# Performance work log

Hardware: AMD Instinct MI355X
Metric: run time of the kernel (lower is better)

The kernel has to match this reference:

```python
import jax, jax.numpy as jnp
import numpy as np
from jax import lax

B, CIN, COUT, K, MOD, BANK = 4, 64, 32, 3, 128, 4
D = H = W = 32
EPS = 1e-8


def _lin_upsample2x(x, axis):
    n = x.shape[axis]
    dst = jnp.arange(2 * n, dtype=jnp.float32)
    src = jnp.maximum((dst + 0.5) * 0.5 - 0.5, 0.0)
    i0 = jnp.floor(src).astype(jnp.int32)
    i1 = jnp.minimum(i0 + 1, n - 1)
    w1 = src - i0.astype(jnp.float32)
    shape = [1] * x.ndim
    shape[axis] = 2 * n
    w1 = w1.reshape(shape)
    return jnp.take(x, i0, axis=axis) * (1.0 - w1) + jnp.take(x, i1, axis=axis) * w1


def upsample_trilinear2x(x):
    for ax in (2, 3, 4):
        x = _lin_upsample2x(x, ax)
    return x


def setup_inputs() -> dict:
    key = jax.random.key(0)
    ks = jax.random.split(key, 9)
    fan = CIN * K * K * K
    return {
        "x": jax.random.normal(ks[0], (B, CIN, D, H, W), jnp.float32),
        "style": jax.random.normal(ks[1], (B, MOD), jnp.float32),
        "bank": jax.random.normal(ks[2], (BANK, COUT, CIN, K, K, K), jnp.float32) / np.sqrt(fan),
        "affine_w": jax.random.normal(ks[3], (CIN, MOD), jnp.float32) / np.sqrt(MOD),
        "affine_b": jnp.ones((CIN,), jnp.float32),  # StyleGAN bias init = 1
        "sel_w": jax.random.normal(ks[4], (BANK, MOD), jnp.float32) / np.sqrt(MOD),
        "sel_b": jnp.zeros((BANK,), jnp.float32),
        "vox_w": jax.random.normal(ks[5], (1, COUT), jnp.float32) / np.sqrt(COUT),
        "vox_b": jnp.zeros((1,), jnp.float32),
    }


def reference(x, style, bank, affine_w, affine_b, sel_w, sel_b, vox_w, vox_b):
    # --- AdaptiveModulatedConv3d: select kernel from bank, modulate, demodulate ---
    alpha = jax.nn.softmax(style @ sel_w.T + sel_b, axis=-1)            # [B, BANK]
    w = jnp.einsum('bn,noidhw->boidhw', alpha, bank)                    # per-sample kernel
    s = style @ affine_w.T + affine_b                                   # [B, CIN]
    w = w * s[:, None, :, None, None, None]                             # modulate
    demod = lax.rsqrt(jnp.sum(w * w, axis=(2, 3, 4, 5)) + EPS)          # [B, COUT]
    w = w * demod[:, :, None, None, None, None]

    def conv1(xi, wi):
        return lax.conv_general_dilated(
            xi[None], wi, window_strides=(1, 1, 1),
            padding=[(1, 1), (1, 1), (1, 1)],
            dimension_numbers=('NCDHW', 'OIDHW', 'NCDHW'))[0]

    y = jax.vmap(conv1)(x, w)                                           # [B, COUT, D, H, W]

    y = upsample_trilinear2x(y)                                         # [B, COUT, 2D, 2H, 2W]

    # --- VoxelizingBlock: 1x1x1 conv to 1 channel ---
    out = jnp.einsum('oc,bcdhw->bodhw', vox_w, y) + vox_b[None, :, None, None, None]
    return (y, out)
```

## Files before the change

### kernel.cpp

```cpp
#include <hip/hip_runtime.h>
#include <math.h>

#define B_    4
#define CIN_  64
#define COUT_ 32
#define MOD_  128
#define VOX_  32768
#define UPVOX_ 262144
#define TAPS_ 27
#define EPS_  1e-8f

#define HALO_   1224
#define XUNITS_ 2448
#define WUNITS_ 1728
#define CHUNK_HALVES_ 13824

#define WS_ALPHA 0
#define WS_S     16
#define WS_WF16  512
#define WS_Y     111104
#define WS_V32   4305408

#define OUT_YUP  0
#define OUT_VOX  33554432

typedef _Float16 half8 __attribute__((ext_vector_type(8)));
typedef float floatx16 __attribute__((ext_vector_type(16)));

__global__ __launch_bounds__(256) void k_style(
    const float* __restrict__ style,
    const float* __restrict__ affine_w,
    const float* __restrict__ affine_b,
    const float* __restrict__ sel_w,
    const float* __restrict__ sel_b,
    float* __restrict__ ws) {
  __shared__ float lg[16];
  const int tid = threadIdx.x;

  if (tid < 16) {
    const int b = tid >> 2, n = tid & 3;
    float l = sel_b[n];
    for (int k = 0; k < MOD_; ++k) l += style[b * MOD_ + k] * sel_w[n * MOD_ + k];
    lg[tid] = l;
  }
  __syncthreads();
  if (tid < 16) {
    const int b = tid >> 2;
    const float m = fmaxf(fmaxf(lg[b * 4 + 0], lg[b * 4 + 1]),
                          fmaxf(lg[b * 4 + 2], lg[b * 4 + 3]));
    float den = 0.f;
    for (int j = 0; j < 4; ++j) den += expf(lg[b * 4 + j] - m);
    ws[WS_ALPHA + tid] = expf(lg[tid] - m) / den;
  }
  {
    const int b = tid >> 6, i = tid & 63;
    float v = affine_b[i];
    for (int k = 0; k < MOD_; ++k) v += style[b * MOD_ + k] * affine_w[i * MOD_ + k];
    ws[WS_S + tid] = v;
  }
}

__global__ __launch_bounds__(256) void k_weights(
    const float* __restrict__ bank,
    const float* __restrict__ ws_in,
    _Float16* __restrict__ wf) {
  const int b = blockIdx.x >> 5;
  const int o = blockIdx.x & 31;
  const int tid = threadIdx.x;
  __shared__ float red[256];

  float al[4];
#pragma unroll
  for (int n = 0; n < 4; ++n) al[n] = ws_in[WS_ALPHA + b * 4 + n];
  const float* sB = ws_in + WS_S + b * 64;

  float wv[7];
  float ss = 0.f;
#pragma unroll
  for (int r = 0; r < 7; ++r) {
    const int e = tid + r * 256;
    float v = 0.f;
    if (e < CIN_ * TAPS_) {
      const int i = e / TAPS_;
      const int t = e - i * TAPS_;
      const int base = (o * CIN_ + i) * TAPS_ + t;
      float bw = 0.f;
#pragma unroll
      for (int n = 0; n < 4; ++n)
        bw += al[n] * bank[base + n * (COUT_ * CIN_ * TAPS_)];
      v = bw * sB[i];
    }
    wv[r] = v;
    ss += v * v;
  }
  red[tid] = ss;
  __syncthreads();
  for (int st = 128; st > 0; st >>= 1) {
    if (tid < st) red[tid] += red[tid + st];
    __syncthreads();
  }
  const float demod = rsqrtf(red[0] + EPS_);

#pragma unroll
  for (int r = 0; r < 7; ++r) {
    const int e = tid + r * 256;
    if (e < CIN_ * TAPS_) {
      const int i = e / TAPS_;
      const int t = e - i * TAPS_;
      const int c = i >> 4, h = (i >> 3) & 1, j = i & 7;
      wf[((((b * 4 + c) * TAPS_ + t) * 2 + h) * 32 + o) * 8 + j] =
          (_Float16)(wv[r] * demod);
    }
  }
}

__global__ __launch_bounds__(256) void k_pack(
    const float* __restrict__ x, _Float16* __restrict__ xt) {
  const int yp = blockIdx.x, zp = blockIdx.y, b = blockIdx.z;
  const int gz = zp - 1, gy = yp - 1;
  const bool zy_ok = ((unsigned)gz < 32u) && ((unsigned)gy < 32u);
  const int gzc = min(max(gz, 0), 31);
  const int gyc = min(max(gy, 0), 31);
  _Float16* dst = xt + (((size_t)(b * 34 + zp) * 34 + yp) * 34) * 64;
  const float* srow = x + ((size_t)b * CIN_) * VOX_ + gzc * 1024 + gyc * 32;
  for (int u = threadIdx.x; u < 34 * 8; u += 256) {
    const int xp = u >> 3, q = u & 7;
    const int gx = xp - 1;
    const bool ok = zy_ok && ((unsigned)gx < 32u);
    const float m = ok ? 1.0f : 0.0f;
    const int gxc = min(max(gx, 0), 31);
    half8 h;
#pragma unroll
    for (int i = 0; i < 8; ++i) {
      const float v = srow[(size_t)(q * 8 + i) * VOX_ + gxc];
      h[i] = (_Float16)(v * m);
    }
    *(half8*)&dst[xp * 64 + q * 8] = h;
  }
}

__global__ __launch_bounds__(256, 1) void k_conv(
    const _Float16* __restrict__ xt,
    const _Float16* __restrict__ wf,
    const float* __restrict__ vox_w,
    float* __restrict__ ws_y,
    float* __restrict__ v32) {
  __shared__ __align__(16) _Float16 wl[2][CHUNK_HALVES_];
  __shared__ __align__(16) _Float16 xs[2][XUNITS_ * 8];

  const int b  = blockIdx.y;
  const int bx = blockIdx.x;
  const int z0 = (bx >> 3) * 4;
  const int y0 = (bx & 7) * 4;
  const int tid = threadIdx.x;
  const int w = tid >> 6;
  const int lane = tid & 63;
  const int hf = lane >> 5;
  const int col = lane & 31;
  const int wz = (w >> 1) * 2;
  const int wy = (w & 1) * 2;

  const _Float16* xtb = xt + (size_t)b * (34 * 34 * 34 * 64);
  const _Float16* wfb = wf + (size_t)b * 4 * CHUNK_HALVES_;

  int xoff[10];
  bool xok[10];
#pragma unroll
  for (int j = 0; j < 10; ++j) {
    const int u = j * 256 + tid;
    xok[j] = (u < XUNITS_);
    const int uc = xok[j] ? u : 0;
    const int h = uc / HALO_, hv = uc - h * HALO_;
    const int hz = hv / 204;
    const int rem = hv - hz * 204;
    const int hy = rem / 34;
    const int hx = rem - hy * 34;
    xoff[j] = (((z0 + hz) * 34 + (y0 + hy)) * 34 + hx) * 64 + h * 8;
  }

  floatx16 acc[2][2];
#pragma unroll
  for (int az = 0; az < 2; ++az)
#pragma unroll
    for (int ay = 0; ay < 2; ++ay)
#pragma unroll
      for (int r = 0; r < 16; ++r) acc[az][ay][r] = 0.f;

  half8 wv[7], xv[10];

  auto load_chunk = [&](int c) {
    const _Float16* wsrc = wfb + (size_t)c * CHUNK_HALVES_;
#pragma unroll
    for (int j = 0; j < 7; ++j) {
      const int u = j * 256 + tid;
      wv[j] = *(const half8*)(wsrc + (size_t)(u < WUNITS_ ? u : 0) * 8);
    }
#pragma unroll
    for (int j = 0; j < 10; ++j)
      xv[j] = *(const half8*)(xtb + xoff[j] + c * 16);
  };
  auto write_chunk = [&](int bufi) {
#pragma unroll
    for (int j = 0; j < 7; ++j) {
      const int u = j * 256 + tid;
      if (u < WUNITS_) *(half8*)&wl[bufi][u * 8] = wv[j];
    }
#pragma unroll
    for (int j = 0; j < 10; ++j) {
      const int u = j * 256 + tid;
      if (xok[j]) *(half8*)&xs[bufi][u * 8] = xv[j];
    }
  };
  auto compute = [&](int bufi) {
    const _Float16* xb_ = xs[bufi];
    const _Float16* wb_ = wl[bufi];
#pragma unroll
    for (int dx = 0; dx < 3; ++dx) {
      half8 Bf[4][4];
#pragma unroll
      for (int zs = 0; zs < 4; ++zs)
#pragma unroll
        for (int ys = 0; ys < 4; ++ys) {
          const int hv = ((wz + zs) * 6 + (wy + ys)) * 34 + dx + col;
          Bf[zs][ys] = *(const half8*)&xb_[(hf * HALO_ + hv) * 8];
        }
#pragma unroll
      for (int dz = 0; dz < 3; ++dz)
#pragma unroll
        for (int dy = 0; dy < 3; ++dy) {
          const int t = (dz * 3 + dy) * 3 + dx;
          const half8 af = *(const half8*)&wb_[((t * 2 + hf) * 32 + col) * 8];
          acc[0][0] = __builtin_amdgcn_mfma_f32_32x32x16_f16(af, Bf[dz][dy], acc[0][0], 0, 0, 0);
          acc[0][1] = __builtin_amdgcn_mfma_f32_32x32x16_f16(af, Bf[dz][dy + 1], acc[0][1], 0, 0, 0);
          acc[1][0] = __builtin_amdgcn_mfma_f32_32x32x16_f16(af, Bf[dz + 1][dy], acc[1][0], 0, 0, 0);
          acc[1][1] = __builtin_amdgcn_mfma_f32_32x32x16_f16(af, Bf[dz + 1][dy + 1], acc[1][1], 0, 0, 0);
        }
    }
  };

  load_chunk(0);
  write_chunk(0);
  __syncthreads();
  for (int c = 0; c < 4; ++c) {
    if (c < 3) load_chunk(c + 1);
    compute(c & 1);
    if (c < 3) {
      write_chunk((c + 1) & 1);
      __syncthreads();
    }
  }

  float vw[16];
#pragma unroll
  for (int r = 0; r < 16; ++r)
    vw[r] = vox_w[(r & 3) + 8 * (r >> 2) + 4 * hf];

  float* yb2 = ws_y + (size_t)b * COUT_ * VOX_;
#pragma unroll
  for (int az = 0; az < 2; ++az)
#pragma unroll
    for (int ay = 0; ay < 2; ++ay) {
      const int zz = z0 + wz + az, yy = y0 + wy + ay;
      const int vbase = zz * 1024 + yy * 32 + col;
      float p = 0.f;
#pragma unroll
      for (int r = 0; r < 16; ++r) {
        const int oc = (r & 3) + 8 * (r >> 2) + 4 * hf;
        yb2[(size_t)oc * VOX_ + vbase] = acc[az][ay][r];
        p = fmaf(vw[r], acc[az][ay][r], p);
      }
      p += __shfl_xor(p, 32);
      if (hf == 0) v32[((size_t)b << 15) + vbase] = p;
    }
}

__global__ __launch_bounds__(256) void k_up(
    const float* __restrict__ ws_y,
    const float* __restrict__ v32,
    const float* __restrict__ vox_b,
    float* __restrict__ out) {
  __shared__ float P[3][1056];
  const int kz = blockIdx.x;
  const int ch = blockIdx.y;
  const int b = blockIdx.z;

  const int pzm = max(kz - 1, 0), pzp = min(kz + 1, 31);
  const float* src = (ch < 32) ? (ws_y + (((size_t)(b * 32 + ch)) << 15))
                               : (v32 + ((size_t)b << 15));
  for (int j = threadIdx.x; j < 768; j += 256) {
    const int p = j >> 8, idx = j & 255;
    const int r = idx >> 3, q = (idx & 7) * 4;
    const int zsrc = (p == 0) ? pzm : ((p == 1) ? kz : pzp);
    const float4 v = *(const float4*)(src + (zsrc << 10) + r * 32 + q);
    float* dp = &P[p][r * 33 + q];
    dp[0] = v.x; dp[1] = v.y; dp[2] = v.z; dp[3] = v.w;
  }
  __syncthreads();

  const int yp = threadIdx.x >> 3;
  const int xq = threadIdx.x & 7;
  const int ym = max(yp - 1, 0) * 33, yc = yp * 33, ypp = min(yp + 1, 31) * 33;

  int gxi[6];
#pragma unroll
  for (int i = 0; i < 6; ++i) gxi[i] = min(max(4 * xq - 1 + i, 0), 31);

  float ry[3][2][6];
#pragma unroll
  for (int p = 0; p < 3; ++p)
#pragma unroll
    for (int i = 0; i < 6; ++i) {
      const float a = P[p][ym + gxi[i]];
      const float bb = P[p][yc + gxi[i]];
      const float cc = P[p][ypp + gxi[i]];
      ry[p][0][i] = fmaf(0.25f, a, 0.75f * bb);
      ry[p][1][i] = fmaf(0.25f, cc, 0.75f * bb);
    }

  const float vb = (ch == 32) ? vox_b[0] : 0.f;
  float* base = out + ((ch < 32) ? (OUT_YUP + (((size_t)(b * 32 + ch)) * UPVOX_))
                                 : (OUT_VOX + (size_t)b * UPVOX_)) +
                (size_t)(2 * kz) * 4096 + (2 * yp) * 64 + 8 * xq;

#pragma unroll
  for (int zo = 0; zo < 2; ++zo)
#pragma unroll
    for (int yo = 0; yo < 2; ++yo) {
      float s[6];
#pragma unroll
      for (int i = 0; i < 6; ++i)
        s[i] = zo == 0 ? fmaf(0.25f, ry[0][yo][i], 0.75f * ry[1][yo][i])
                       : fmaf(0.25f, ry[2][yo][i], 0.75f * ry[1][yo][i]);
      float o[8];
#pragma unroll
      for (int ox = 0; ox < 8; ++ox) {
        const int k = ox >> 1;
        o[ox] = (ox & 1) ? fmaf(0.25f, s[k + 2], 0.75f * s[k + 1])
                         : fmaf(0.25f, s[k], 0.75f * s[k + 1]);
        o[ox] += vb;
      }
      float4* dst = (float4*)(base + (size_t)zo * 4096 + yo * 64);
      float4 v0; v0.x = o[0]; v0.y = o[1]; v0.z = o[2]; v0.w = o[3];
      float4 v1; v1.x = o[4]; v1.y = o[5]; v1.z = o[6]; v1.w = o[7];
      dst[0] = v0;
      dst[1] = v1;
    }
}

extern "C" void kernel_launch(void* const* d_in, const int* in_sizes, int n_in,
                              void* d_out, int out_size, void* d_ws, size_t ws_size,
                              hipStream_t stream) {
  const float* x        = (const float*)d_in[0];
  const float* style    = (const float*)d_in[1];
  const float* bank     = (const float*)d_in[2];
  const float* affine_w = (const float*)d_in[3];
  const float* affine_b = (const float*)d_in[4];
  const float* sel_w    = (const float*)d_in[5];
  const float* sel_b    = (const float*)d_in[6];
  const float* vox_w    = (const float*)d_in[7];
  const float* vox_b    = (const float*)d_in[8];
  float* out = (float*)d_out;
  float* ws  = (float*)d_ws;
  _Float16* wf16 = (_Float16*)(ws + WS_WF16);
  float* ws_y = ws + WS_Y;
  float* v32  = ws + WS_V32;
  _Float16* xt = (_Float16*)d_out;

  k_style<<<1, 256, 0, stream>>>(style, affine_w, affine_b, sel_w, sel_b, ws);
  k_weights<<<128, 256, 0, stream>>>(bank, ws, wf16);
  k_pack<<<dim3(34, 34, B_), 256, 0, stream>>>(x, xt);
  k_conv<<<dim3(64, B_), 256, 0, stream>>>(xt, wf16, vox_w, ws_y, v32);
  k_up<<<dim3(32, 33, B_), 256, 0, stream>>>(ws_y, v32, vox_b, out);
}
```

Measured before the change: 235.1 us.

## Fuse prep kernels, load conv weights to registers, widen upsample blocks

Merges the style, weight-modulation and input-pack kernels into one launch, with the modulation done by extra blocks in a fifth z-slice, cutting two launches and the serial dependency between them. In the conv kernel, each lane now reads its 27 weight fragments straight from global into registers instead of staging the weights through shared memory, which frees LDS but adds register pressure. The upsample kernel now handles two source z-slices per block, reusing the loaded planes, and writes its output with nontemporal stores.

```diff
diff --git a/kernel.cpp b/kernel.cpp
--- a/kernel.cpp
+++ b/kernel.cpp
@@ -12,11 +12,8 @@
 
 #define HALO_   1224
 #define XUNITS_ 2448
-#define WUNITS_ 1728
 #define CHUNK_HALVES_ 13824
 
-#define WS_ALPHA 0
-#define WS_S     16
 #define WS_WF16  512
 #define WS_Y     111104
 #define WS_V32   4305408
@@ -26,96 +23,95 @@
 
 typedef _Float16 half8 __attribute__((ext_vector_type(8)));
 typedef float floatx16 __attribute__((ext_vector_type(16)));
-
-__global__ __launch_bounds__(256) void k_style(
+typedef float floatx4 __attribute__((ext_vector_type(4)));
+
+__global__ __launch_bounds__(256) void k_prep(
+    const float* __restrict__ x,
     const float* __restrict__ style,
+    const float* __restrict__ bank,
     const float* __restrict__ affine_w,
     const float* __restrict__ affine_b,
     const float* __restrict__ sel_w,
     const float* __restrict__ sel_b,
-    float* __restrict__ ws) {
-  __shared__ float lg[16];
+    _Float16* __restrict__ xt,
+    _Float16* __restrict__ wf) {
+  __shared__ float red[256];
+  __shared__ float sS[64];
+  __shared__ float sLg[4];
+  __shared__ float sAl[4];
   const int tid = threadIdx.x;
 
-  if (tid < 16) {
-    const int b = tid >> 2, n = tid & 3;
-    float l = sel_b[n];
-    for (int k = 0; k < MOD_; ++k) l += style[b * MOD_ + k] * sel_w[n * MOD_ + k];
-    lg[tid] = l;
-  }
-  __syncthreads();
-  if (tid < 16) {
-    const int b = tid >> 2;
-    const float m = fmaxf(fmaxf(lg[b * 4 + 0], lg[b * 4 + 1]),
-                          fmaxf(lg[b * 4 + 2], lg[b * 4 + 3]));
-    float den = 0.f;
-    for (int j = 0; j < 4; ++j) den += expf(lg[b * 4 + j] - m);
-    ws[WS_ALPHA + tid] = expf(lg[tid] - m) / den;
-  }
-  {
-    const int b = tid >> 6, i = tid & 63;
-    float v = affine_b[i];
-    for (int k = 0; k < MOD_; ++k) v += style[b * MOD_ + k] * affine_w[i * MOD_ + k];
-    ws[WS_S + tid] = v;
-  }
-}
-
-__global__ __launch_bounds__(256) void k_weights(
-    const float* __restrict__ bank,
-    const float* __restrict__ ws_in,
-    _Float16* __restrict__ wf) {
-  const int b = blockIdx.x >> 5;
-  const int o = blockIdx.x & 31;
-  const int tid = threadIdx.x;
-  __shared__ float red[256];
-
-  float al[4];
-#pragma unroll
-  for (int n = 0; n < 4; ++n) al[n] = ws_in[WS_ALPHA + b * 4 + n];
-  const float* sB = ws_in + WS_S + b * 64;
-
-  float wv[7];
-  float ss = 0.f;
-#pragma unroll
-  for (int r = 0; r < 7; ++r) {
-    const int e = tid + r * 256;
-    float v = 0.f;
-    if (e < CIN_ * TAPS_) {
-      const int i = e / TAPS_;
-      const int t = e - i * TAPS_;
-      const int base = (o * CIN_ + i) * TAPS_ + t;
-      float bw = 0.f;
-#pragma unroll
-      for (int n = 0; n < 4; ++n)
-        bw += al[n] * bank[base + n * (COUT_ * CIN_ * TAPS_)];
-      v = bw * sB[i];
-    }
-    wv[r] = v;
-    ss += v * v;
-  }
-  red[tid] = ss;
-  __syncthreads();
-  for (int st = 128; st > 0; st >>= 1) {
-    if (tid < st) red[tid] += red[tid + st];
+  if (blockIdx.z == 4) {
+    const int sid = blockIdx.y * 34 + blockIdx.x;
+    if (sid >= 128) return;
+    const int b = sid >> 5;
+    const int o = sid & 31;
+    const float* st = style + b * MOD_;
+
+    if (tid < 64) {
+      float v = affine_b[tid];
+      for (int k = 0; k < MOD_; ++k) v += st[k] * affine_w[tid * MOD_ + k];
+      sS[tid] = v;
+    } else if (tid < 68) {
+      const int n = tid - 64;
+      float l = sel_b[n];
+      for (int k = 0; k < MOD_; ++k) l += st[k] * sel_w[n * MOD_ + k];
+      sLg[n] = l;
+    }
     __syncthreads();
-  }
-  const float demod = rsqrtf(red[0] + EPS_);
-
-#pragma unroll
-  for (int r = 0; r < 7; ++r) {
-    const int e = tid + r * 256;
-    if (e < CIN_ * TAPS_) {
-      const int i = e / TAPS_;
-      const int t = e - i * TAPS_;
-      const int c = i >> 4, h = (i >> 3) & 1, j = i & 7;
-      wf[((((b * 4 + c) * TAPS_ + t) * 2 + h) * 32 + o) * 8 + j] =
-          (_Float16)(wv[r] * demod);
-    }
-  }
-}
-
-__global__ __launch_bounds__(256) void k_pack(
-    const float* __restrict__ x, _Float16* __restrict__ xt) {
+    if (tid < 4) {
+      const float m = fmaxf(fmaxf(sLg[0], sLg[1]), fmaxf(sLg[2], sLg[3]));
+      float den = 0.f;
+      for (int j = 0; j < 4; ++j) den += expf(sLg[j] - m);
+      sAl[tid] = expf(sLg[tid] - m) / den;
+    }
+    __syncthreads();
+
+    float al[4];
+#pragma unroll
+    for (int n = 0; n < 4; ++n) al[n] = sAl[n];
+
+    float wv[7];
+    float ss = 0.f;
+#pragma unroll
+    for (int r = 0; r < 7; ++r) {
+      const int e = tid + r * 256;
+      float v = 0.f;
+      if (e < CIN_ * TAPS_) {
+        const int i = e / TAPS_;
+        const int t = e - i * TAPS_;
+        const int base = (o * CIN_ + i) * TAPS_ + t;
+        float bw = 0.f;
+#pragma unroll
+        for (int n = 0; n < 4; ++n)
+          bw += al[n] * bank[base + n * (COUT_ * CIN_ * TAPS_)];
+        v = bw * sS[i];
+      }
+      wv[r] = v;
+      ss += v * v;
+    }
+    red[tid] = ss;
+    __syncthreads();
+    for (int stg = 128; stg > 0; stg >>= 1) {
+      if (tid < stg) red[tid] += red[tid + stg];
+      __syncthreads();
+    }
+    const float demod = rsqrtf(red[0] + EPS_);
+
+#pragma unroll
+    for (int r = 0; r < 7; ++r) {
+      const int e = tid + r * 256;
+      if (e < CIN_ * TAPS_) {
+        const int i = e / TAPS_;
+        const int t = e - i * TAPS_;
+        const int c = i >> 4, h = (i >> 3) & 1, j = i & 7;
+        wf[((((b * 4 + c) * TAPS_ + t) * 2 + h) * 32 + o) * 8 + j] =
+            (_Float16)(wv[r] * demod);
+      }
+    }
+    return;
+  }
+
   const int yp = blockIdx.x, zp = blockIdx.y, b = blockIdx.z;
   const int gz = zp - 1, gy = yp - 1;
   const bool zy_ok = ((unsigned)gz < 32u) && ((unsigned)gy < 32u);
@@ -123,7 +119,7 @@
   const int gyc = min(max(gy, 0), 31);
   _Float16* dst = xt + (((size_t)(b * 34 + zp) * 34 + yp) * 34) * 64;
   const float* srow = x + ((size_t)b * CIN_) * VOX_ + gzc * 1024 + gyc * 32;
-  for (int u = threadIdx.x; u < 34 * 8; u += 256) {
+  for (int u = tid; u < 34 * 8; u += 256) {
     const int xp = u >> 3, q = u & 7;
     const int gx = xp - 1;
     const bool ok = zy_ok && ((unsigned)gx < 32u);
@@ -145,7 +141,6 @@
     const float* __restrict__ vox_w,
     float* __restrict__ ws_y,
     float* __restrict__ v32) {
-  __shared__ __align__(16) _Float16 wl[2][CHUNK_HALVES_];
   __shared__ __align__(16) _Float16 xs[2][XUNITS_ * 8];
 
   const int b  = blockIdx.y;
@@ -162,6 +157,7 @@
 
   const _Float16* xtb = xt + (size_t)b * (34 * 34 * 34 * 64);
   const _Float16* wfb = wf + (size_t)b * 4 * CHUNK_HALVES_;
+  const _Float16* wlane = wfb + ((size_t)(hf * 32 + col)) * 8;
 
   int xoff[10];
   bool xok[10];
@@ -186,26 +182,20 @@
 #pragma unroll
       for (int r = 0; r < 16; ++r) acc[az][ay][r] = 0.f;
 
-  half8 wv[7], xv[10];
-
+  half8 xv[10], afv[27];
+
+  auto load_af = [&](int c) {
+#pragma unroll
+    for (int t = 0; t < TAPS_; ++t)
+      afv[t] = *(const half8*)(wlane + (size_t)c * CHUNK_HALVES_ + t * 512);
+  };
   auto load_chunk = [&](int c) {
-    const _Float16* wsrc = wfb + (size_t)c * CHUNK_HALVES_;
-#pragma unroll
-    for (int j = 0; j < 7; ++j) {
-      const int u = j * 256 + tid;
-      wv[j] = *(const half8*)(wsrc + (size_t)(u < WUNITS_ ? u : 0) * 8);
-    }
 #pragma unroll
     for (int j = 0; j < 10; ++j)
       xv[j] = *(const half8*)(xtb + xoff[j] + c * 16);
   };
   auto write_chunk = [&](int bufi) {
 #pragma unroll
-    for (int j = 0; j < 7; ++j) {
-      const int u = j * 256 + tid;
-      if (u < WUNITS_) *(half8*)&wl[bufi][u * 8] = wv[j];
-    }
-#pragma unroll
     for (int j = 0; j < 10; ++j) {
       const int u = j * 256 + tid;
       if (xok[j]) *(half8*)&xs[bufi][u * 8] = xv[j];
@@ -213,7 +203,6 @@
   };
   auto compute = [&](int bufi) {
     const _Float16* xb_ = xs[bufi];
-    const _Float16* wb_ = wl[bufi];
 #pragma unroll
     for (int dx = 0; dx < 3; ++dx) {
       half8 Bf[4][4];
@@ -228,8 +217,7 @@
       for (int dz = 0; dz < 3; ++dz)
 #pragma unroll
         for (int dy = 0; dy < 3; ++dy) {
-          const int t = (dz * 3 + dy) * 3 + dx;
-          const half8 af = *(const half8*)&wb_[((t * 2 + hf) * 32 + col) * 8];
+          const half8 af = afv[(dz * 3 + dy) * 3 + dx];
           acc[0][0] = __builtin_amdgcn_mfma_f32_32x32x16_f16(af, Bf[dz][dy], acc[0][0], 0, 0, 0);
           acc[0][1] = __builtin_amdgcn_mfma_f32_32x32x16_f16(af, Bf[dz][dy + 1], acc[0][1], 0, 0, 0);
           acc[1][0] = __builtin_amdgcn_mfma_f32_32x32x16_f16(af, Bf[dz + 1][dy], acc[1][0], 0, 0, 0);
@@ -238,6 +226,7 @@
     }
   };
 
+  load_af(0);
   load_chunk(0);
   write_chunk(0);
   __syncthreads();
@@ -245,6 +234,7 @@
     if (c < 3) load_chunk(c + 1);
     compute(c & 1);
     if (c < 3) {
+      load_af(c + 1);
       write_chunk((c + 1) & 1);
       __syncthreads();
     }
@@ -279,18 +269,17 @@
     const float* __restrict__ v32,
     const float* __restrict__ vox_b,
     float* __restrict__ out) {
-  __shared__ float P[3][1056];
-  const int kz = blockIdx.x;
+  __shared__ float P[4][1056];
+  const int kq = blockIdx.x;
   const int ch = blockIdx.y;
   const int b = blockIdx.z;
 
-  const int pzm = max(kz - 1, 0), pzp = min(kz + 1, 31);
   const float* src = (ch < 32) ? (ws_y + (((size_t)(b * 32 + ch)) << 15))
                                : (v32 + ((size_t)b << 15));
-  for (int j = threadIdx.x; j < 768; j += 256) {
+  for (int j = threadIdx.x; j < 1024; j += 256) {
     const int p = j >> 8, idx = j & 255;
     const int r = idx >> 3, q = (idx & 7) * 4;
-    const int zsrc = (p == 0) ? pzm : ((p == 1) ? kz : pzp);
+    const int zsrc = min(max(2 * kq - 1 + p, 0), 31);
     const float4 v = *(const float4*)(src + (zsrc << 10) + r * 32 + q);
     float* dp = &P[p][r * 33 + q];
     dp[0] = v.x; dp[1] = v.y; dp[2] = v.z; dp[3] = v.w;
@@ -305,46 +294,50 @@
 #pragma unroll
   for (int i = 0; i < 6; ++i) gxi[i] = min(max(4 * xq - 1 + i, 0), 31);
 
-  float ry[3][2][6];
-#pragma unroll
-  for (int p = 0; p < 3; ++p)
-#pragma unroll
-    for (int i = 0; i < 6; ++i) {
-      const float a = P[p][ym + gxi[i]];
-      const float bb = P[p][yc + gxi[i]];
-      const float cc = P[p][ypp + gxi[i]];
-      ry[p][0][i] = fmaf(0.25f, a, 0.75f * bb);
-      ry[p][1][i] = fmaf(0.25f, cc, 0.75f * bb);
-    }
-
   const float vb = (ch == 32) ? vox_b[0] : 0.f;
-  float* base = out + ((ch < 32) ? (OUT_YUP + (((size_t)(b * 32 + ch)) * UPVOX_))
-                                 : (OUT_VOX + (size_t)b * UPVOX_)) +
-                (size_t)(2 * kz) * 4096 + (2 * yp) * 64 + 8 * xq;
-
-#pragma unroll
-  for (int zo = 0; zo < 2; ++zo)
-#pragma unroll
-    for (int yo = 0; yo < 2; ++yo) {
-      float s[6];
-#pragma unroll
-      for (int i = 0; i < 6; ++i)
-        s[i] = zo == 0 ? fmaf(0.25f, ry[0][yo][i], 0.75f * ry[1][yo][i])
-                       : fmaf(0.25f, ry[2][yo][i], 0.75f * ry[1][yo][i]);
-      float o[8];
-#pragma unroll
-      for (int ox = 0; ox < 8; ++ox) {
-        const int k = ox >> 1;
-        o[ox] = (ox & 1) ? fmaf(0.25f, s[k + 2], 0.75f * s[k + 1])
-                         : fmaf(0.25f, s[k], 0.75f * s[k + 1]);
-        o[ox] += vb;
-      }
-      float4* dst = (float4*)(base + (size_t)zo * 4096 + yo * 64);
-      float4 v0; v0.x = o[0]; v0.y = o[1]; v0.z = o[2]; v0.w = o[3];
-      float4 v1; v1.x = o[4]; v1.y = o[5]; v1.z = o[6]; v1.w = o[7];
-      dst[0] = v0;
-      dst[1] = v1;
-    }
+  float* base0 = out + ((ch < 32) ? (OUT_YUP + (((size_t)(b * 32 + ch)) * UPVOX_))
+                                  : (OUT_VOX + (size_t)b * UPVOX_)) +
+                 (2 * yp) * 64 + 8 * xq;
+
+#pragma unroll
+  for (int zi = 0; zi < 2; ++zi) {
+    float ry[3][2][6];
+#pragma unroll
+    for (int p = 0; p < 3; ++p)
+#pragma unroll
+      for (int i = 0; i < 6; ++i) {
+        const float a = P[zi + p][ym + gxi[i]];
+        const float bb = P[zi + p][yc + gxi[i]];
+        const float cc = P[zi + p][ypp + gxi[i]];
+        ry[p][0][i] = fmaf(0.25f, a, 0.75f * bb);
+        ry[p][1][i] = fmaf(0.25f, cc, 0.75f * bb);
+      }
+
+    float* base = base0 + (size_t)(2 * (2 * kq + zi)) * 4096;
+#pragma unroll
+    for (int zo = 0; zo < 2; ++zo)
+#pragma unroll
+      for (int yo = 0; yo < 2; ++yo) {
+        float s[6];
+#pragma unroll
+        for (int i = 0; i < 6; ++i)
+          s[i] = zo == 0 ? fmaf(0.25f, ry[0][yo][i], 0.75f * ry[1][yo][i])
+                         : fmaf(0.25f, ry[2][yo][i], 0.75f * ry[1][yo][i]);
+        float o[8];
+#pragma unroll
+        for (int ox = 0; ox < 8; ++ox) {
+          const int k = ox >> 1;
+          o[ox] = (ox & 1) ? fmaf(0.25f, s[k + 2], 0.75f * s[k + 1])
+                           : fmaf(0.25f, s[k], 0.75f * s[k + 1]);
+          o[ox] += vb;
+        }
+        float* dst = base + (size_t)zo * 4096 + yo * 64;
+        floatx4 v0; v0.x = o[0]; v0.y = o[1]; v0.z = o[2]; v0.w = o[3];
+        floatx4 v1; v1.x = o[4]; v1.y = o[5]; v1.z = o[6]; v1.w = o[7];
+        __builtin_nontemporal_store(v0, (floatx4*)dst);
+        __builtin_nontemporal_store(v1, (floatx4*)(dst + 4));
+      }
+  }
 }
 
 extern "C" void kernel_launch(void* const* d_in, const int* in_sizes, int n_in,
@@ -366,9 +359,8 @@
   float* v32  = ws + WS_V32;
   _Float16* xt = (_Float16*)d_out;
 
-  k_style<<<1, 256, 0, stream>>>(style, affine_w, affine_b, sel_w, sel_b, ws);
-  k_weights<<<128, 256, 0, stream>>>(bank, ws, wf16);
-  k_pack<<<dim3(34, 34, B_), 256, 0, stream>>>(x, xt);
+  k_prep<<<dim3(34, 34, 5), 256, 0, stream>>>(x, style, bank, affine_w, affine_b,
+                                              sel_w, sel_b, xt, wf16);
   k_conv<<<dim3(64, B_), 256, 0, stream>>>(xt, wf16, vox_w, ws_y, v32);
-  k_up<<<dim3(32, 33, B_), 256, 0, stream>>>(ws_y, v32, vox_b, out);
+  k_up<<<dim3(16, 33, B_), 256, 0, stream>>>(ws_y, v32, vox_b, out);
 }
```

Measured after the change: 258.7 us. 1.1x slower.
